# Performance work log

Hardware: AMD Instinct MI355X
Metric: run time of the kernel (lower is better)

The kernel has to match this reference:

```python
import jax, jax.numpy as jnp
import numpy as np

NOISE_LEVEL = 1.0

def setup_inputs() -> dict:
    key = jax.random.key(0)
    k1, k2, k3 = jax.random.split(key, 3)
    N, NUM_CODE, DIM_CODE = 16384, 2048, 512
    x = jax.random.normal(k1, (N, NUM_CODE), dtype=jnp.float32)
    noise = jax.random.uniform(k2, (N, NUM_CODE), dtype=jnp.float32)
    codebook = jax.random.normal(k3, (NUM_CODE, DIM_CODE), dtype=jnp.float32)
    return {"x": x, "noise": noise, "codebook": codebook}

def reference(x, noise, codebook):
    # softmax over codes
    sm = jax.nn.softmax(x, axis=1)                      # [N, num_code]
    # noisy argmax (noise replaces torch.rand_like for determinism)
    idx = jnp.argmax(sm - NOISE_LEVEL * noise, axis=1)  # [N]
    one_hot = jax.nn.one_hot(idx, x.shape[1], dtype=sm.dtype)
    # straight-through: value == one_hot, gradient flows through softmax
    ste = sm - jax.lax.stop_gradient(sm - one_hot)
    y = ste @ codebook                                   # [N, dim_code]
    return y
```

## Files before the change

kernel.cpp:

```cpp
#include <hip/hip_runtime.h>

#define NUM_CODE 2048
#define DIM_CODE 512

__global__ __launch_bounds__(256) void vq_row_kernel(
    const float* __restrict__ x,
    const float* __restrict__ noise,
    const float* __restrict__ codebook,
    float* __restrict__ out)
{
    const int tid  = threadIdx.x;
    const int lane = tid & 63;
    const int wave = tid >> 6;
    const int row  = blockIdx.x * 4 + wave;

    const float4* x4 = (const float4*)(x     + (size_t)row * NUM_CODE);
    const float4* n4 = (const float4*)(noise + (size_t)row * NUM_CODE);

    float4 a[8];
    float4 nz[8];
    #pragma unroll
    for (int j = 0; j < 8; ++j) a[j]  = x4[j * 64 + lane];
    #pragma unroll
    for (int j = 0; j < 8; ++j) nz[j] = n4[j * 64 + lane];
    __builtin_amdgcn_sched_barrier(0);

    float m = fmaxf(fmaxf(a[0].x, a[0].y), fmaxf(a[0].z, a[0].w));
    #pragma unroll
    for (int j = 1; j < 8; ++j)
        m = fmaxf(m, fmaxf(fmaxf(a[j].x, a[j].y), fmaxf(a[j].z, a[j].w)));
    #pragma unroll
    for (int off = 32; off; off >>= 1)
        m = fmaxf(m, __shfl_xor(m, off));

    float s = 0.f;
    #pragma unroll
    for (int j = 0; j < 8; ++j) {
        a[j].x = expf(a[j].x - m);
        a[j].y = expf(a[j].y - m);
        a[j].z = expf(a[j].z - m);
        a[j].w = expf(a[j].w - m);
        s += (a[j].x + a[j].y) + (a[j].z + a[j].w);
    }
    #pragma unroll
    for (int off = 32; off; off >>= 1)
        s += __shfl_xor(s, off);
    const float inv = 1.0f / s;

    float bv = -INFINITY; int bi = 0;
    #pragma unroll
    for (int j = 0; j < 8; ++j) {
        const int base = 256 * j + 4 * lane;
        { float v = a[j].x * inv - nz[j].x; if (v > bv) { bv = v; bi = base;     } }
        { float v = a[j].y * inv - nz[j].y; if (v > bv) { bv = v; bi = base + 1; } }
        { float v = a[j].z * inv - nz[j].z; if (v > bv) { bv = v; bi = base + 2; } }
        { float v = a[j].w * inv - nz[j].w; if (v > bv) { bv = v; bi = base + 3; } }
    }
    #pragma unroll
    for (int off = 32; off; off >>= 1) {
        float ov = __shfl_xor(bv, off);
        int   oi = __shfl_xor(bi, off);
        if (ov > bv || (ov == bv && oi < bi)) { bv = ov; bi = oi; }
    }

    const float4* cb = (const float4*)(codebook + (size_t)bi * DIM_CODE);
    float4*       o  = (float4*)(out + (size_t)row * DIM_CODE);
    o[lane]      = cb[lane];
    o[64 + lane] = cb[64 + lane];
}

extern "C" void kernel_launch(void* const* d_in, const int* in_sizes, int n_in,
                              void* d_out, int out_size, void* d_ws, size_t ws_size,
                              hipStream_t stream) {
    const float* x        = (const float*)d_in[0];
    const float* noise    = (const float*)d_in[1];
    const float* codebook = (const float*)d_in[2];
    float* out            = (float*)d_out;

    const int n_rows = in_sizes[0] / NUM_CODE;
    vq_row_kernel<<<n_rows / 4, 256, 0, stream>>>(x, noise, codebook, out);
}
```

Before: 56.01 us.

## Process four rows per wave with double-buffered register prefetch

Each wave now handles four consecutive rows and uses two register buffers, so loads for the next row are issued before the current row is processed. The grid shrinks fourfold, and launch bounds ask for three blocks per SIMD-level occupancy hint. The aim is to hide global load latency in this memory-bound kernel. In exchange each thread holds about twice as many registers, which lowers occupancy, and there are fewer blocks across the CUs.

```diff
diff --git a/kernel.cpp b/kernel.cpp
--- a/kernel.cpp
+++ b/kernel.cpp
@@ -3,32 +3,29 @@
 #define NUM_CODE 2048
 #define DIM_CODE 512
 
-__global__ __launch_bounds__(256) void vq_row_kernel(
-    const float* __restrict__ x,
-    const float* __restrict__ noise,
-    const float* __restrict__ codebook,
-    float* __restrict__ out)
-{
-    const int tid  = threadIdx.x;
-    const int lane = tid & 63;
-    const int wave = tid >> 6;
-    const int row  = blockIdx.x * 4 + wave;
 
-    const float4* x4 = (const float4*)(x     + (size_t)row * NUM_CODE);
-    const float4* n4 = (const float4*)(noise + (size_t)row * NUM_CODE);
+struct RowBuf {
+    float4 x[8];
+    float4 n[8];
+};
 
-    float4 a[8];
-    float4 nz[8];
+__device__ __forceinline__ void issue_loads(RowBuf& b, const float* __restrict__ xrow,
+                                            const float* __restrict__ nrow, int lane) {
+    const float4* x4 = (const float4*)xrow;
+    const float4* n4 = (const float4*)nrow;
     #pragma unroll
-    for (int j = 0; j < 8; ++j) a[j]  = x4[j * 64 + lane];
+    for (int j = 0; j < 8; ++j) b.x[j] = x4[j * 64 + lane];
     #pragma unroll
-    for (int j = 0; j < 8; ++j) nz[j] = n4[j * 64 + lane];
-    __builtin_amdgcn_sched_barrier(0);
+    for (int j = 0; j < 8; ++j) b.n[j] = n4[j * 64 + lane];
+}
 
-    float m = fmaxf(fmaxf(a[0].x, a[0].y), fmaxf(a[0].z, a[0].w));
+__device__ __forceinline__ void process_row(RowBuf& b, int lane,
+                                            const float* __restrict__ codebook,
+                                            float* __restrict__ orow) {
+    float m = fmaxf(fmaxf(b.x[0].x, b.x[0].y), fmaxf(b.x[0].z, b.x[0].w));
     #pragma unroll
     for (int j = 1; j < 8; ++j)
-        m = fmaxf(m, fmaxf(fmaxf(a[j].x, a[j].y), fmaxf(a[j].z, a[j].w)));
+        m = fmaxf(m, fmaxf(fmaxf(b.x[j].x, b.x[j].y), fmaxf(b.x[j].z, b.x[j].w)));
     #pragma unroll
     for (int off = 32; off; off >>= 1)
         m = fmaxf(m, __shfl_xor(m, off));
@@ -36,11 +33,11 @@
     float s = 0.f;
     #pragma unroll
     for (int j = 0; j < 8; ++j) {
-        a[j].x = expf(a[j].x - m);
-        a[j].y = expf(a[j].y - m);
-        a[j].z = expf(a[j].z - m);
-        a[j].w = expf(a[j].w - m);
-        s += (a[j].x + a[j].y) + (a[j].z + a[j].w);
+        b.x[j].x = expf(b.x[j].x - m);
+        b.x[j].y = expf(b.x[j].y - m);
+        b.x[j].z = expf(b.x[j].z - m);
+        b.x[j].w = expf(b.x[j].w - m);
+        s += (b.x[j].x + b.x[j].y) + (b.x[j].z + b.x[j].w);
     }
     #pragma unroll
     for (int off = 32; off; off >>= 1)
@@ -51,10 +48,10 @@
     #pragma unroll
     for (int j = 0; j < 8; ++j) {
         const int base = 256 * j + 4 * lane;
-        { float v = a[j].x * inv - nz[j].x; if (v > bv) { bv = v; bi = base;     } }
-        { float v = a[j].y * inv - nz[j].y; if (v > bv) { bv = v; bi = base + 1; } }
-        { float v = a[j].z * inv - nz[j].z; if (v > bv) { bv = v; bi = base + 2; } }
-        { float v = a[j].w * inv - nz[j].w; if (v > bv) { bv = v; bi = base + 3; } }
+        { float v = b.x[j].x * inv - b.n[j].x; if (v > bv) { bv = v; bi = base;     } }
+        { float v = b.x[j].y * inv - b.n[j].y; if (v > bv) { bv = v; bi = base + 1; } }
+        { float v = b.x[j].z * inv - b.n[j].z; if (v > bv) { bv = v; bi = base + 2; } }
+        { float v = b.x[j].w * inv - b.n[j].w; if (v > bv) { bv = v; bi = base + 3; } }
     }
     #pragma unroll
     for (int off = 32; off; off >>= 1) {
@@ -64,9 +61,38 @@
     }
 
     const float4* cb = (const float4*)(codebook + (size_t)bi * DIM_CODE);
-    float4*       o  = (float4*)(out + (size_t)row * DIM_CODE);
+    float4* o = (float4*)orow;
     o[lane]      = cb[lane];
     o[64 + lane] = cb[64 + lane];
+}
+
+__global__ __launch_bounds__(256, 3) void vq_row_kernel(
+    const float* __restrict__ x,
+    const float* __restrict__ noise,
+    const float* __restrict__ codebook,
+    float* __restrict__ out)
+{
+    const int tid  = threadIdx.x;
+    const int lane = tid & 63;
+    const int wave = tid >> 6;
+    const size_t r0 = ((size_t)blockIdx.x * 4 + wave) * 4;
+
+    RowBuf A, B;
+    issue_loads(A, x + r0 * NUM_CODE, noise + r0 * NUM_CODE, lane);
+    __builtin_amdgcn_sched_barrier(0);
+    issue_loads(B, x + (r0 + 1) * NUM_CODE, noise + (r0 + 1) * NUM_CODE, lane);
+    __builtin_amdgcn_sched_barrier(0);
+
+    process_row(A, lane, codebook, out + r0 * DIM_CODE);
+    issue_loads(A, x + (r0 + 2) * NUM_CODE, noise + (r0 + 2) * NUM_CODE, lane);
+    __builtin_amdgcn_sched_barrier(0);
+
+    process_row(B, lane, codebook, out + (r0 + 1) * DIM_CODE);
+    issue_loads(B, x + (r0 + 3) * NUM_CODE, noise + (r0 + 3) * NUM_CODE, lane);
+    __builtin_amdgcn_sched_barrier(0);
+
+    process_row(A, lane, codebook, out + (r0 + 2) * DIM_CODE);
+    process_row(B, lane, codebook, out + (r0 + 3) * DIM_CODE);
 }
 
 extern "C" void kernel_launch(void* const* d_in, const int* in_sizes, int n_in,
@@ -77,6 +103,8 @@
     const float* codebook = (const float*)d_in[2];
     float* out            = (float*)d_out;
 
-    const int n_rows = in_sizes[0] / NUM_CODE;
-    vq_row_kernel<<<n_rows / 4, 256, 0, stream>>>(x, noise, codebook, out);
+    const int n_rows  = in_sizes[0] / NUM_CODE;
+    const int n_blocks = n_rows / (4 * 4);
+
+    vq_row_kernel<<<n_blocks, 256, 0, stream>>>(x, noise, codebook, out);
 }
```

Result: slower. 70.23 us (+25.4%).
